# Kernel tuning notes

Hardware: AMD Instinct MI355X
Metric: run time of the kernel (lower is better)

Reference implementation:

```python
import jax, jax.numpy as jnp
import numpy as np

H = 2048          # hidden_size
I = 1024          # moe_intermediate_size
E = 32            # n_routed_experts
K = 4             # num_experts_per_tok
N_SHARED = 1
EPS = 1e-6


def setup_inputs() -> dict:
    key = jax.random.key(0)
    ks = jax.random.split(key, 8)
    s = 1.0 / np.sqrt(H)
    si = 1.0 / np.sqrt(I)
    return {
        "hidden_states": jax.random.normal(ks[0], (1, 4096, H), jnp.float32),
        "norm_w": jnp.ones((H,), jnp.float32),
        "gate_w": jax.random.normal(ks[1], (E, H), jnp.float32) * s,      # MoEGate.weight
        "w13": jax.random.normal(ks[2], (E, H, 2 * I), jnp.float32) * s,  # fused w1w3
        "w2": jax.random.normal(ks[3], (E, I, H), jnp.float32) * si,      # fused w2
        "shared_gate_w": jax.random.normal(ks[4], (H, I * N_SHARED), jnp.float32) * s,
        "shared_up_w": jax.random.normal(ks[5], (H, I * N_SHARED), jnp.float32) * s,
        "shared_down_w": jax.random.normal(ks[6], (I * N_SHARED, H), jnp.float32) * si,
    }


def _rmsnorm(x, w, eps=EPS):
    var = jnp.mean(jnp.square(x), axis=-1, keepdims=True)
    return x * jax.lax.rsqrt(var + eps) * w


def _moe_core(x, gate_w, w13, w2):
    # x: [T, H] (post-norm tokens)
    T = x.shape[0]
    N = T * K
    C = 2 * N // E

    # --- gate (fp32, F.linear) ---
    logits = jnp.einsum("th,eh->te", x.astype(jnp.float32), gate_w.astype(jnp.float32))
    scores = jax.nn.softmax(logits, axis=-1)
    topk_w, topk_ids = jax.lax.top_k(scores, K)           # [T, K]
    topk_w = topk_w / jnp.sum(topk_w, axis=-1, keepdims=True)  # norm_topk_prob

    # --- dispatch: sort token-expert pairs by expert ---
    flat_ids = topk_ids.reshape(-1)                        # [N] int
    flat_w = topk_w.reshape(-1)                            # [N]
    order = jnp.argsort(flat_ids)                          # stable sort by expert
    sorted_eid = flat_ids[order]                           # [N]
    tok = order // K                                       # source token per sorted slot
    counts = jnp.zeros((E,), jnp.int32).at[flat_ids].add(1)  # tokens_per_expert
    starts = jnp.cumsum(counts) - counts
    pos = jnp.arange(N) - starts[sorted_eid]               # position within expert group

    # scatter tokens into [E, C, H] buffer (OOB rows dropped; C sized so this ~never happens)
    buf = jnp.zeros((E, C, x.shape[1]), x.dtype).at[sorted_eid, pos].set(x[tok], mode="drop")

    # --- grouped expert FFN (swiglu) ---
    gu = jnp.einsum("ech,ehf->ecf", buf, w13)              # [E, C, 2I]
    g, u = jnp.split(gu, 2, axis=-1)
    act = jax.nn.silu(g) * u                               # swiglu
    eo = jnp.einsum("eci,eih->ech", act, w2)               # [E, C, H]

    # --- combine: gather back and weighted scatter-add per source token ---
    out_slots = eo[sorted_eid, pos]                        # [N, H]
    routed = jnp.zeros_like(x).at[tok].add(out_slots * flat_w[order][:, None])
    return routed


def reference(hidden_states, norm_w, gate_w, w13, w2, shared_gate_w, shared_up_w, shared_down_w):
    B, S, Hd = hidden_states.shape
    residual = hidden_states
    h = _rmsnorm(hidden_states, norm_w)                    # post_attention_layernorm
    x = h.reshape(-1, Hd)                                  # [T, H]

    routed = _moe_core(x, gate_w, w13, w2)                 # routed experts output

    # shared experts MLP (swiglu)
    shared = (jax.nn.silu(x @ shared_gate_w) * (x @ shared_up_w)) @ shared_down_w

    out = residual + (routed + shared).reshape(B, S, Hd)
    return out
```

## Files before the change

kernel.cpp:

```cpp
#include <hip/hip_runtime.h>
#include <hip/hip_bf16.h>
#include <math.h>

#define HD 2048
#define ID 1024
#define NE 32
#define TOPK 4
#define NTOK 4096
#define NSLOT (NTOK*TOPK)

typedef __attribute__((ext_vector_type(4))) float f32x4;
typedef __attribute__((ext_vector_type(8))) short bf16x8;
typedef unsigned short u16;
typedef unsigned int u32;

union U32x4BF { uint4 u; bf16x8 h; };

static __device__ __forceinline__ u16 f2bf(float f) {
  union { float f; u32 u; } v; v.f = f;
  u32 r = v.u + 0x7fffu + ((v.u >> 16) & 1u);
  return (u16)(r >> 16);
}

static __device__ __forceinline__ u32 cvtpk(float lo, float hi) {
  u32 r;
  asm("v_cvt_pk_bf16_f32 %0, %1, %2" : "=v"(r) : "v"(lo), "v"(hi));
  return r;
}

static __device__ __forceinline__ void barrier_lgkm() {
  asm volatile("s_waitcnt lgkmcnt(0)" ::: "memory");
  __builtin_amdgcn_s_barrier();
}

__global__ __launch_bounds__(256) void k_rmsnorm(const float* __restrict__ x,
                                                 const float* __restrict__ w,
                                                 u16* __restrict__ xn) {
  int t = blockIdx.x, tid = threadIdx.x;
  const float* row = x + (size_t)t * HD;
  float4 v0 = ((const float4*)row)[tid*2+0];
  float4 v1 = ((const float4*)row)[tid*2+1];
  float ss = v0.x*v0.x+v0.y*v0.y+v0.z*v0.z+v0.w*v0.w
           + v1.x*v1.x+v1.y*v1.y+v1.z*v1.z+v1.w*v1.w;
  #pragma unroll
  for (int d=1; d<64; d<<=1) ss += __shfl_xor(ss, d);
  __shared__ float red[4];
  if ((tid&63)==0) red[tid>>6] = ss;
  __syncthreads();
  float rs = rsqrtf((red[0]+red[1]+red[2]+red[3]) * (1.0f/HD) + 1e-6f);
  const float* wp = w + tid*8;
  float a[8] = {v0.x,v0.y,v0.z,v0.w,v1.x,v1.y,v1.z,v1.w};
  uint4 o;
  o.x = (u32)f2bf(a[0]*rs*wp[0]) | ((u32)f2bf(a[1]*rs*wp[1])<<16);
  o.y = (u32)f2bf(a[2]*rs*wp[2]) | ((u32)f2bf(a[3]*rs*wp[3])<<16);
  o.z = (u32)f2bf(a[4]*rs*wp[4]) | ((u32)f2bf(a[5]*rs*wp[5])<<16);
  o.w = (u32)f2bf(a[6]*rs*wp[6]) | ((u32)f2bf(a[7]*rs*wp[7])<<16);
  ((uint4*)xn)[(size_t)t*(HD/8) + tid] = o;
}

__global__ __launch_bounds__(256) void k_gate(const float* __restrict__ x,
                                              const float* __restrict__ w,
                                              const float* __restrict__ gw,
                                              int* __restrict__ topk_id,
                                              float* __restrict__ topk_w,
                                              int* __restrict__ counts) {
  __shared__ float xs[HD];
  __shared__ float red[4];
  __shared__ float logits[NE];
  int t = blockIdx.x, tid = threadIdx.x;
  const float* row = x + (size_t)t*HD;
  float4 v0 = ((const float4*)row)[tid*2+0];
  float4 v1 = ((const float4*)row)[tid*2+1];
  float ss = v0.x*v0.x+v0.y*v0.y+v0.z*v0.z+v0.w*v0.w
           + v1.x*v1.x+v1.y*v1.y+v1.z*v1.z+v1.w*v1.w;
  #pragma unroll
  for (int d=1; d<64; d<<=1) ss += __shfl_xor(ss, d);
  if ((tid&63)==0) red[tid>>6] = ss;
  __syncthreads();
  float rs = 1.0f / sqrtf((red[0]+red[1]+red[2]+red[3]) * (1.0f/HD) + 1e-6f);
  const float* wp = w + tid*8;
  float a[8] = {v0.x,v0.y,v0.z,v0.w,v1.x,v1.y,v1.z,v1.w};
  #pragma unroll
  for (int j=0;j<8;++j) xs[tid*8+j] = a[j]*rs*wp[j];
  __syncthreads();
  int wave = tid>>6, lane = tid&63;
  for (int ei=0; ei<8; ++ei) {
    int e = wave*8 + ei;
    const float* g = gw + (size_t)e*HD;
    float s = 0.f;
    #pragma unroll
    for (int j=0;j<HD/64;++j) s += xs[lane + j*64] * g[lane + j*64];
    #pragma unroll
    for (int d=1; d<64; d<<=1) s += __shfl_xor(s, d);
    if (lane==0) logits[e] = s;
  }
  __syncthreads();
  if (tid==0) {
    float best[TOPK]; int bid[TOPK]; unsigned used = 0;
    for (int k2=0;k2<TOPK;++k2) {
      float bv = -1e30f; int bi = 0;
      for (int i2=0;i2<NE;++i2)
        if (!((used>>i2)&1u) && logits[i2] > bv) { bv = logits[i2]; bi = i2; }
      used |= 1u<<bi; best[k2] = bv; bid[k2] = bi;
    }
    float mx = best[0], sum = 0.f, wv[TOPK];
    for (int k2=0;k2<TOPK;++k2) { wv[k2] = expf(best[k2]-mx); sum += wv[k2]; }
    float inv = 1.f/sum;
    for (int k2=0;k2<TOPK;++k2) {
      topk_id[t*TOPK+k2] = bid[k2];
      topk_w[t*TOPK+k2] = wv[k2]*inv;
      atomicAdd(&counts[bid[k2]], 1);
    }
  }
}

__global__ void k_zero(int* counts, int* cursors) {
  int i = threadIdx.x;
  if (i < NE) { counts[i] = 0; cursors[i] = 0; }
}

__global__ void k_scan(const int* __restrict__ counts, int* __restrict__ starts) {
  if (threadIdx.x==0 && blockIdx.x==0) {
    int acc = 0;
    for (int e=0;e<NE;++e) { starts[e] = acc; acc += counts[e]; }
  }
}

__global__ __launch_bounds__(256) void k_dispatch(const int* __restrict__ topk_id,
                                                  const float* __restrict__ topk_w,
                                                  const int* __restrict__ starts,
                                                  int* __restrict__ cursors,
                                                  int* __restrict__ slot_tok,
                                                  float* __restrict__ slot_w) {
  int i = blockIdx.x*256 + threadIdx.x;
  int e = topk_id[i];
  int p = atomicAdd(&cursors[e], 1);
  int slot = starts[e] + p;
  slot_tok[slot] = i >> 2;
  slot_w[slot] = topk_w[i];
}

template<bool INDEXED>
__global__ __launch_bounds__(256) void k_gemm_up(
    const u16* __restrict__ A, int lda, int kiter,
    const float* __restrict__ Bg, const float* __restrict__ Bu,
    size_t bstride, int ldb,
    const int* __restrict__ counts, const int* __restrict__ starts,
    const int* __restrict__ slot_tok,
    u16* __restrict__ actOut) {
  __shared__ u16 Al[2][4096];
  __shared__ u16 Bl[2][4096];
  __shared__ int rowL[128];
  int t = threadIdx.x;
  int n0 = blockIdx.x * 64;
  int m0 = blockIdx.y * 128;
  int e  = blockIdx.z;
  int M, rowbase;
  if (INDEXED) { M = counts[e]; rowbase = starts[e]; if (m0 >= M) return; }
  else { M = NTOK; rowbase = 0; }
  if (t < 128) {
    int m = m0 + t;
    rowL[t] = INDEXED ? slot_tok[rowbase + (m < M ? m : M-1)] : m;
  }
  __syncthreads();
  int r0i = t>>2, r1i = r0i + 64;
  int segA = ((t&3) ^ ((r0i>>1)&3)) << 3;
  const u16* srcA0 = A + (size_t)rowL[r0i]*lda + segA;
  const u16* srcA1 = A + (size_t)rowL[r1i]*lda + segA;
  int sc4 = (t&31)*4;
  int kb  = t>>5;
  int isup = (sc4>>4)&1;
  int srccol = n0 + ((sc4>>5)<<4) + (sc4&15);
  const float* bsrc = (isup ? Bu : Bg) + (INDEXED ? (size_t)e*bstride : 0)
                    + (size_t)(kb*4)*ldb + srccol;
  int bq4 = (kb ^ (t&7))*4;

  int lane = t&63, wave = t>>6, wr = wave>>1, wc = wave&1;
  int l15 = lane&15, l4 = lane>>4;
  int aoff[4], b0off[4], b1off[4];
  #pragma unroll
  for (int f=0; f<4; ++f) {
    int r = wr*64 + f*16 + l15;
    aoff[f] = r*32 + ((l4 ^ ((r>>1)&3))<<3);
    int c = wc*64 + f*16 + l15;
    int g = (c>>2)&7;
    b0off[f] = c*32 + (((2*l4)   ^ g)<<2);
    b1off[f] = c*32 + (((2*l4+1) ^ g)<<2);
  }
  f32x4 acc[4][4];
  #pragma unroll
  for (int fm=0;fm<4;++fm)
    #pragma unroll
    for (int fn=0;fn<4;++fn)
      acc[fm][fn] = (f32x4){0.f,0.f,0.f,0.f};

  uint4 av0 = *(const uint4*)srcA0;
  uint4 av1 = *(const uint4*)srcA1;
  float4 bv[4];
  #pragma unroll
  for (int i=0;i<4;++i) bv[i] = *(const float4*)(bsrc + (size_t)i*ldb);
  srcA0 += 32; srcA1 += 32; bsrc += (size_t)32*ldb;
  *(uint4*)&Al[0][t*8] = av0;
  *(uint4*)&Al[0][2048 + t*8] = av1;
  {
    const float* f0 = (const float*)&bv[0];
    const float* f1 = (const float*)&bv[1];
    const float* f2 = (const float*)&bv[2];
    const float* f3 = (const float*)&bv[3];
    #pragma unroll
    for (int j=0;j<4;++j) {
      uint2 wv; wv.x = cvtpk(f0[j], f1[j]); wv.y = cvtpk(f2[j], f3[j]);
      *(uint2*)&Bl[0][(sc4+j)*32 + bq4] = wv;
    }
  }
  barrier_lgkm();

  int cur = 0;
  for (int kt = 0; kt < kiter; ++kt) {
    bool more = (kt+1 < kiter);
    uint4 avn0, avn1; float4 bvn[4];
    if (more) {
      avn0 = *(const uint4*)srcA0;
      avn1 = *(const uint4*)srcA1;
      #pragma unroll
      for (int i=0;i<4;++i) bvn[i] = *(const float4*)(bsrc + (size_t)i*ldb);
      srcA0 += 32; srcA1 += 32; bsrc += (size_t)32*ldb;
    }
    bf16x8 af[4], bfr[4];
    #pragma unroll
    for (int f=0; f<4; ++f) af[f] = *(const bf16x8*)&Al[cur][aoff[f]];
    #pragma unroll
    for (int f=0; f<4; ++f) {
      uint2 lo = *(const uint2*)&Bl[cur][b0off[f]];
      uint2 hi = *(const uint2*)&Bl[cur][b1off[f]];
      U32x4BF ub; ub.u = make_uint4(lo.x, lo.y, hi.x, hi.y);
      bfr[f] = ub.h;
    }
    #pragma unroll
    for (int fm=0; fm<4; ++fm)
      #pragma unroll
      for (int fn=0; fn<4; ++fn)
        acc[fm][fn] = __builtin_amdgcn_mfma_f32_16x16x32_bf16(af[fm], bfr[fn], acc[fm][fn], 0,0,0);
    if (more) {
      *(uint4*)&Al[cur^1][t*8] = avn0;
      *(uint4*)&Al[cur^1][2048 + t*8] = avn1;
      const float* f0 = (const float*)&bvn[0];
      const float* f1 = (const float*)&bvn[1];
      const float* f2 = (const float*)&bvn[2];
      const float* f3 = (const float*)&bvn[3];
      #pragma unroll
      for (int j=0;j<4;++j) {
        uint2 wv; wv.x = cvtpk(f0[j], f1[j]); wv.y = cvtpk(f2[j], f3[j]);
        *(uint2*)&Bl[cur^1][(sc4+j)*32 + bq4] = wv;
      }
    }
    cur ^= 1;
    barrier_lgkm();
  }
  #pragma unroll
  for (int fm=0; fm<4; ++fm) {
    #pragma unroll
    for (int fq=0; fq<2; ++fq) {
      f32x4 g = acc[fm][2*fq], u = acc[fm][2*fq+1];
      int col = n0 + (wc*2+fq)*16 + l15;
      #pragma unroll
      for (int r=0;r<4;++r) {
        int mloc = wr*64 + fm*16 + l4*4 + r;
        int m = m0 + mloc;
        if (m < M) {
          float gv = g[r];
          float av = gv / (1.f + expf(-gv)) * u[r];
          actOut[(size_t)(rowbase+m)*ID + col] = f2bf(av);
        }
      }
    }
  }
}

template<bool INDEXED>
__global__ __launch_bounds__(256) void k_gemm_down(
    const u16* __restrict__ A, int lda, int kiter,
    const float* __restrict__ B, size_t bstride, int ldb,
    const int* __restrict__ counts, const int* __restrict__ starts,
    const int* __restrict__ slot_tok, const float* __restrict__ slot_w,
    const float* __restrict__ resid,
    float* __restrict__ out) {
  __shared__ u16 Al[2][4096];
  __shared__ u16 Bl[2][4096];
  __shared__ int tokL[128];
  __shared__ float wL[128];
  int t = threadIdx.x;
  int n0 = blockIdx.x * 128;
  int m0 = blockIdx.y * 128;
  int e  = blockIdx.z;
  int M, rowbase;
  if (INDEXED) { M = counts[e]; rowbase = starts[e]; if (m0 >= M) return; }
  else { M = NTOK; rowbase = 0; }
  if (INDEXED && t < 128) {
    int m = m0 + t;
    tokL[t] = (m<M) ? slot_tok[rowbase+m] : 0;
    wL[t]   = (m<M) ? slot_w[rowbase+m]  : 0.f;
  }
  if (INDEXED) __syncthreads();
  int r0i = t>>2, r1i = r0i + 64;
  int segA = ((t&3) ^ ((r0i>>1)&3)) << 3;
  int am0 = m0 + r0i, am1 = m0 + r1i;
  const u16* srcA0 = A + (size_t)(rowbase + (am0 < M ? am0 : M-1))*lda + segA;
  const u16* srcA1 = A + (size_t)(rowbase + (am1 < M ? am1 : M-1))*lda + segA;
  int sc4 = (t&31)*4;
  int kb  = t>>5;
  const float* bsrc = B + (INDEXED ? (size_t)e*bstride : 0)
                    + (size_t)(kb*4)*ldb + (n0 + sc4);
  int bq4 = (kb ^ (t&7))*4;

  int lane = t&63, wave = t>>6, wr = wave>>1, wc = wave&1;
  int l15 = lane&15, l4 = lane>>4;
  int aoff[4], b0off[4], b1off[4];
  #pragma unroll
  for (int f=0; f<4; ++f) {
    int r = wr*64 + f*16 + l15;
    aoff[f] = r*32 + ((l4 ^ ((r>>1)&3))<<3);
    int c = wc*64 + f*16 + l15;
    int g = (c>>2)&7;
    b0off[f] = c*32 + (((2*l4)   ^ g)<<2);
    b1off[f] = c*32 + (((2*l4+1) ^ g)<<2);
  }
  f32x4 acc[4][4];
  #pragma unroll
  for (int fm=0;fm<4;++fm)
    #pragma unroll
    for (int fn=0;fn<4;++fn)
      acc[fm][fn] = (f32x4){0.f,0.f,0.f,0.f};

  uint4 av0 = *(const uint4*)srcA0;
  uint4 av1 = *(const uint4*)srcA1;
  float4 bv[4];
  #pragma unroll
  for (int i=0;i<4;++i) bv[i] = *(const float4*)(bsrc + (size_t)i*ldb);
  srcA0 += 32; srcA1 += 32; bsrc += (size_t)32*ldb;
  *(uint4*)&Al[0][t*8] = av0;
  *(uint4*)&Al[0][2048 + t*8] = av1;
  {
    const float* f0 = (const float*)&bv[0];
    const float* f1 = (const float*)&bv[1];
    const float* f2 = (const float*)&bv[2];
    const float* f3 = (const float*)&bv[3];
    #pragma unroll
    for (int j=0;j<4;++j) {
      uint2 wv; wv.x = cvtpk(f0[j], f1[j]); wv.y = cvtpk(f2[j], f3[j]);
      *(uint2*)&Bl[0][(sc4+j)*32 + bq4] = wv;
    }
  }
  barrier_lgkm();

  int cur = 0;
  for (int kt = 0; kt < kiter; ++kt) {
    bool more = (kt+1 < kiter);
    uint4 avn0, avn1; float4 bvn[4];
    if (more) {
      avn0 = *(const uint4*)srcA0;
      avn1 = *(const uint4*)srcA1;
      #pragma unroll
      for (int i=0;i<4;++i) bvn[i] = *(const float4*)(bsrc + (size_t)i*ldb);
      srcA0 += 32; srcA1 += 32; bsrc += (size_t)32*ldb;
    }
    bf16x8 af[4], bfr[4];
    #pragma unroll
    for (int f=0; f<4; ++f) af[f] = *(const bf16x8*)&Al[cur][aoff[f]];
    #pragma unroll
    for (int f=0; f<4; ++f) {
      uint2 lo = *(const uint2*)&Bl[cur][b0off[f]];
      uint2 hi = *(const uint2*)&Bl[cur][b1off[f]];
      U32x4BF ub; ub.u = make_uint4(lo.x, lo.y, hi.x, hi.y);
      bfr[f] = ub.h;
    }
    #pragma unroll
    for (int fm=0; fm<4; ++fm)
      #pragma unroll
      for (int fn=0; fn<4; ++fn)
        acc[fm][fn] = __builtin_amdgcn_mfma_f32_16x16x32_bf16(af[fm], bfr[fn], acc[fm][fn], 0,0,0);
    if (more) {
      *(uint4*)&Al[cur^1][t*8] = avn0;
      *(uint4*)&Al[cur^1][2048 + t*8] = avn1;
      const float* f0 = (const float*)&bvn[0];
      const float* f1 = (const float*)&bvn[1];
      const float* f2 = (const float*)&bvn[2];
      const float* f3 = (const float*)&bvn[3];
      #pragma unroll
      for (int j=0;j<4;++j) {
        uint2 wv; wv.x = cvtpk(f0[j], f1[j]); wv.y = cvtpk(f2[j], f3[j]);
        *(uint2*)&Bl[cur^1][(sc4+j)*32 + bq4] = wv;
      }
    }
    cur ^= 1;
    barrier_lgkm();
  }
  #pragma unroll
  for (int fm=0; fm<4; ++fm) {
    #pragma unroll
    for (int fn=0; fn<4; ++fn) {
      f32x4 v = acc[fm][fn];
      int col = n0 + wc*64 + fn*16 + l15;
      #pragma unroll
      for (int r=0;r<4;++r) {
        int mloc = wr*64 + fm*16 + l4*4 + r;
        int m = m0 + mloc;
        if (m < M) {
          if (INDEXED) {
            atomicAdd(&out[(size_t)tokL[mloc]*HD + col], v[r]*wL[mloc]);
          } else {
            size_t o = (size_t)m*HD + col;
            out[o] = resid[o] + v[r];
          }
        }
      }
    }
  }
}

extern "C" void kernel_launch(void* const* d_in, const int* in_sizes, int n_in,
                              void* d_out, int out_size, void* d_ws, size_t ws_size,
                              hipStream_t stream) {
  const float* x    = (const float*)d_in[0];
  const float* nw   = (const float*)d_in[1];
  const float* gw   = (const float*)d_in[2];
  const float* w13  = (const float*)d_in[3];
  const float* w2   = (const float*)d_in[4];
  const float* sgw  = (const float*)d_in[5];
  const float* suw  = (const float*)d_in[6];
  const float* sdw  = (const float*)d_in[7];
  float* out = (float*)d_out;

  char* p = (char*)d_ws;
  u16* xn   = (u16*)p;  p += (size_t)NTOK*HD*2;
  u16* act  = (u16*)p;  p += (size_t)NSLOT*ID*2;
  u16* sact = (u16*)p;  p += (size_t)NTOK*ID*2;
  int*   topk_id  = (int*)p;   p += (size_t)NTOK*TOPK*4;
  float* topk_w   = (float*)p; p += (size_t)NTOK*TOPK*4;
  int*   slot_tok = (int*)p;   p += (size_t)NSLOT*4;
  float* slot_w   = (float*)p; p += (size_t)NSLOT*4;
  int*   counts   = (int*)p;   p += 64*4;
  int*   cursors  = (int*)p;   p += 64*4;
  int*   starts   = (int*)p;   p += 64*4;

  k_zero<<<1, 64, 0, stream>>>(counts, cursors);
  k_rmsnorm<<<NTOK, 256, 0, stream>>>(x, nw, xn);
  k_gate<<<NTOK, 256, 0, stream>>>(x, nw, gw, topk_id, topk_w, counts);
  k_scan<<<1, 1, 0, stream>>>(counts, starts);
  k_dispatch<<<NSLOT/256, 256, 0, stream>>>(topk_id, topk_w, starts, cursors, slot_tok, slot_w);

  k_gemm_up<true><<<dim3(ID/64, 8, NE), 256, 0, stream>>>(
      xn, HD, HD/32, w13, w13 + ID, (size_t)HD*2*ID, 2*ID,
      counts, starts, slot_tok, act);
  k_gemm_up<false><<<dim3(ID/64, NTOK/128, 1), 256, 0, stream>>>(
      xn, HD, HD/32, sgw, suw, 0, ID, nullptr, nullptr, nullptr, sact);
  k_gemm_down<false><<<dim3(HD/128, NTOK/128, 1), 256, 0, stream>>>(
      sact, ID, ID/32, sdw, 0, HD, nullptr, nullptr, nullptr, nullptr, x, out);
  k_gemm_down<true><<<dim3(HD/128, 8, NE), 256, 0, stream>>>(
      act, ID, ID/32, w2, (size_t)ID*HD, HD, counts, starts, slot_tok, slot_w, nullptr, out);
}
```

Before: 792.2 us.

## Double N tile width in MoE GEMMs with per-wave column split and new LDS swizzle

New measurement: 869.6 us. 9.8% more time.

```diff
diff --git a/kernel.cpp b/kernel.cpp
--- a/kernel.cpp
+++ b/kernel.cpp
@@ -140,8 +140,31 @@
   slot_w[slot] = topk_w[i];
 }
 
+static __device__ __forceinline__ void packB(u16* Bb, int tq, int kb, const float4* bv) {
+  int h = tq & 15;
+  #pragma unroll
+  for (int j = 0; j < 4; ++j) {
+    int p = 2*tq + (j>>1);
+    int cpar = j & 1;
+    int s0 = ((4*kb + 0 + cpar) ^ h) * 4;
+    int s1 = ((4*kb + 2 + cpar) ^ h) * 4;
+    uint2 w0, w1;
+    w0.x = cvtpk(((const float*)&bv[0])[j], ((const float*)&bv[1])[j]);
+    w0.y = cvtpk(((const float*)&bv[2])[j], ((const float*)&bv[3])[j]);
+    w1.x = cvtpk(((const float*)&bv[4])[j], ((const float*)&bv[5])[j]);
+    w1.y = cvtpk(((const float*)&bv[6])[j], ((const float*)&bv[7])[j]);
+    *(uint2*)&Bb[p*64 + s0] = w0;
+    *(uint2*)&Bb[p*64 + s1] = w1;
+  }
+}
+
+static __device__ __forceinline__ void loadB8(const float* bsrc, int ldb, float4* bv) {
+  #pragma unroll
+  for (int i = 0; i < 8; ++i) bv[i] = *(const float4*)(bsrc + (size_t)i*ldb);
+}
+
 template<bool INDEXED>
-__global__ __launch_bounds__(256) void k_gemm_up(
+__global__ __launch_bounds__(256, 2) void k_gemm_up(
     const u16* __restrict__ A, int lda, int kiter,
     const float* __restrict__ Bg, const float* __restrict__ Bu,
     size_t bstride, int ldb,
@@ -149,10 +172,10 @@
     const int* __restrict__ slot_tok,
     u16* __restrict__ actOut) {
   __shared__ u16 Al[2][4096];
-  __shared__ u16 Bl[2][4096];
+  __shared__ u16 Bl[2][8192];
   __shared__ int rowL[128];
   int t = threadIdx.x;
-  int n0 = blockIdx.x * 64;
+  int n0 = blockIdx.x * 128;
   int m0 = blockIdx.y * 128;
   int e  = blockIdx.z;
   int M, rowbase;
@@ -163,109 +186,86 @@
     rowL[t] = INDEXED ? slot_tok[rowbase + (m < M ? m : M-1)] : m;
   }
   __syncthreads();
-  int r0i = t>>2, r1i = r0i + 64;
+  int r0i = t>>2;
   int segA = ((t&3) ^ ((r0i>>1)&3)) << 3;
   const u16* srcA0 = A + (size_t)rowL[r0i]*lda + segA;
-  const u16* srcA1 = A + (size_t)rowL[r1i]*lda + segA;
-  int sc4 = (t&31)*4;
-  int kb  = t>>5;
-  int isup = (sc4>>4)&1;
-  int srccol = n0 + ((sc4>>5)<<4) + (sc4&15);
+  const u16* srcA1 = A + (size_t)rowL[r0i+64]*lda + segA;
+  int tq = t & 63, kb = t >> 6;
+  int sc4 = tq * 4;
+  int isup = (sc4 >> 4) & 1;
+  int og = ((sc4 >> 5) << 4) | (sc4 & 15);
   const float* bsrc = (isup ? Bu : Bg) + (INDEXED ? (size_t)e*bstride : 0)
-                    + (size_t)(kb*4)*ldb + srccol;
-  int bq4 = (kb ^ (t&7))*4;
-
-  int lane = t&63, wave = t>>6, wr = wave>>1, wc = wave&1;
+                    + (size_t)(kb*8)*ldb + (n0 + og);
+
+  int lane = t&63, wn = t>>6;
   int l15 = lane&15, l4 = lane>>4;
-  int aoff[4], b0off[4], b1off[4];
-  #pragma unroll
-  for (int f=0; f<4; ++f) {
-    int r = wr*64 + f*16 + l15;
-    aoff[f] = r*32 + ((l4 ^ ((r>>1)&3))<<3);
-    int c = wc*64 + f*16 + l15;
-    int g = (c>>2)&7;
-    b0off[f] = c*32 + (((2*l4)   ^ g)<<2);
-    b1off[f] = c*32 + (((2*l4+1) ^ g)<<2);
-  }
-  f32x4 acc[4][4];
-  #pragma unroll
-  for (int fm=0;fm<4;++fm)
+  int aoffb = l15*32 + ((l4 ^ ((l15>>1)&3))<<3);
+  int b0off[4];
+  #pragma unroll
+  for (int fn=0; fn<4; ++fn) {
+    int pbase = wn*32 + fn*8 + (l15>>1);
+    int h = (fn*4 + (l15>>2)) & 15;
+    b0off[fn] = pbase*64 + (((4*l4 + (l15&1)) ^ h) << 2);
+  }
+  f32x4 acc[8][4];
+  #pragma unroll
+  for (int fm=0;fm<8;++fm)
     #pragma unroll
     for (int fn=0;fn<4;++fn)
       acc[fm][fn] = (f32x4){0.f,0.f,0.f,0.f};
 
-  uint4 av0 = *(const uint4*)srcA0;
-  uint4 av1 = *(const uint4*)srcA1;
-  float4 bv[4];
-  #pragma unroll
-  for (int i=0;i<4;++i) bv[i] = *(const float4*)(bsrc + (size_t)i*ldb);
+  uint4 aA0 = *(const uint4*)srcA0, aA1 = *(const uint4*)srcA1;
+  float4 bv[8]; loadB8(bsrc, ldb, bv);
   srcA0 += 32; srcA1 += 32; bsrc += (size_t)32*ldb;
-  *(uint4*)&Al[0][t*8] = av0;
-  *(uint4*)&Al[0][2048 + t*8] = av1;
-  {
-    const float* f0 = (const float*)&bv[0];
-    const float* f1 = (const float*)&bv[1];
-    const float* f2 = (const float*)&bv[2];
-    const float* f3 = (const float*)&bv[3];
-    #pragma unroll
-    for (int j=0;j<4;++j) {
-      uint2 wv; wv.x = cvtpk(f0[j], f1[j]); wv.y = cvtpk(f2[j], f3[j]);
-      *(uint2*)&Bl[0][(sc4+j)*32 + bq4] = wv;
-    }
-  }
+  *(uint4*)&Al[0][t*8] = aA0;
+  *(uint4*)&Al[0][2048 + t*8] = aA1;
+  packB(Bl[0], tq, kb, bv);
   barrier_lgkm();
 
   int cur = 0;
   for (int kt = 0; kt < kiter; ++kt) {
     bool more = (kt+1 < kiter);
-    uint4 avn0, avn1; float4 bvn[4];
     if (more) {
-      avn0 = *(const uint4*)srcA0;
-      avn1 = *(const uint4*)srcA1;
-      #pragma unroll
-      for (int i=0;i<4;++i) bvn[i] = *(const float4*)(bsrc + (size_t)i*ldb);
+      aA0 = *(const uint4*)srcA0; aA1 = *(const uint4*)srcA1;
+      loadB8(bsrc, ldb, bv);
       srcA0 += 32; srcA1 += 32; bsrc += (size_t)32*ldb;
     }
-    bf16x8 af[4], bfr[4];
-    #pragma unroll
-    for (int f=0; f<4; ++f) af[f] = *(const bf16x8*)&Al[cur][aoff[f]];
-    #pragma unroll
-    for (int f=0; f<4; ++f) {
-      uint2 lo = *(const uint2*)&Bl[cur][b0off[f]];
-      uint2 hi = *(const uint2*)&Bl[cur][b1off[f]];
-      U32x4BF ub; ub.u = make_uint4(lo.x, lo.y, hi.x, hi.y);
-      bfr[f] = ub.h;
-    }
-    #pragma unroll
-    for (int fm=0; fm<4; ++fm)
-      #pragma unroll
-      for (int fn=0; fn<4; ++fn)
-        acc[fm][fn] = __builtin_amdgcn_mfma_f32_16x16x32_bf16(af[fm], bfr[fn], acc[fm][fn], 0,0,0);
+    {
+      bf16x8 bfr[4];
+      #pragma unroll
+      for (int fn=0; fn<4; ++fn) {
+        uint2 lo = *(const uint2*)&Bl[cur][b0off[fn]];
+        uint2 hi = *(const uint2*)&Bl[cur][b0off[fn] ^ 8];
+        U32x4BF ub; ub.u = make_uint4(lo.x, lo.y, hi.x, hi.y);
+        bfr[fn] = ub.h;
+      }
+      __builtin_amdgcn_s_setprio(1);
+      #pragma unroll
+      for (int fm=0; fm<8; ++fm) {
+        bf16x8 af = *(const bf16x8*)&Al[cur][aoffb + fm*512];
+        #pragma unroll
+        for (int fn=0; fn<4; ++fn)
+          acc[fm][fn] = __builtin_amdgcn_mfma_f32_16x16x32_bf16(af, bfr[fn], acc[fm][fn], 0,0,0);
+      }
+      __builtin_amdgcn_s_setprio(0);
+    }
     if (more) {
-      *(uint4*)&Al[cur^1][t*8] = avn0;
-      *(uint4*)&Al[cur^1][2048 + t*8] = avn1;
-      const float* f0 = (const float*)&bvn[0];
-      const float* f1 = (const float*)&bvn[1];
-      const float* f2 = (const float*)&bvn[2];
-      const float* f3 = (const float*)&bvn[3];
-      #pragma unroll
-      for (int j=0;j<4;++j) {
-        uint2 wv; wv.x = cvtpk(f0[j], f1[j]); wv.y = cvtpk(f2[j], f3[j]);
-        *(uint2*)&Bl[cur^1][(sc4+j)*32 + bq4] = wv;
-      }
+      *(uint4*)&Al[cur^1][t*8] = aA0;
+      *(uint4*)&Al[cur^1][2048 + t*8] = aA1;
+      packB(Bl[cur^1], tq, kb, bv);
     }
     cur ^= 1;
     barrier_lgkm();
   }
   #pragma unroll
-  for (int fm=0; fm<4; ++fm) {
+  for (int fm=0; fm<8; ++fm) {
     #pragma unroll
     for (int fq=0; fq<2; ++fq) {
       f32x4 g = acc[fm][2*fq], u = acc[fm][2*fq+1];
-      int col = n0 + (wc*2+fq)*16 + l15;
+      int col = n0 + (wn*2+fq)*16 + l15;
       #pragma unroll
       for (int r=0;r<4;++r) {
-        int mloc = wr*64 + fm*16 + l4*4 + r;
+        int mloc = fm*16 + l4*4 + r;
         int m = m0 + mloc;
         if (m < M) {
           float gv = g[r];
@@ -278,7 +278,7 @@
 }
 
 template<bool INDEXED>
-__global__ __launch_bounds__(256) void k_gemm_down(
+__global__ __launch_bounds__(256, 2) void k_gemm_down(
     const u16* __restrict__ A, int lda, int kiter,
     const float* __restrict__ B, size_t bstride, int ldb,
     const int* __restrict__ counts, const int* __restrict__ starts,
@@ -286,11 +286,11 @@
     const float* __restrict__ resid,
     float* __restrict__ out) {
   __shared__ u16 Al[2][4096];
-  __shared__ u16 Bl[2][4096];
+  __shared__ u16 Bl[2][8192];
   __shared__ int tokL[128];
   __shared__ float wL[128];
   int t = threadIdx.x;
-  int n0 = blockIdx.x * 128;
+  int n0 = blockIdx.x * 256;
   int m0 = blockIdx.y * 128;
   int e  = blockIdx.z;
   int M, rowbase;
@@ -302,108 +302,85 @@
     wL[t]   = (m<M) ? slot_w[rowbase+m]  : 0.f;
   }
   if (INDEXED) __syncthreads();
-  int r0i = t>>2, r1i = r0i + 64;
+  int r0i = t>>2;
   int segA = ((t&3) ^ ((r0i>>1)&3)) << 3;
-  int am0 = m0 + r0i, am1 = m0 + r1i;
+  int am0 = m0 + r0i, am1 = m0 + r0i + 64;
   const u16* srcA0 = A + (size_t)(rowbase + (am0 < M ? am0 : M-1))*lda + segA;
   const u16* srcA1 = A + (size_t)(rowbase + (am1 < M ? am1 : M-1))*lda + segA;
-  int sc4 = (t&31)*4;
-  int kb  = t>>5;
+  int tq = t & 63, kb = t >> 6;
+  int sc4 = tq * 4;
   const float* bsrc = B + (INDEXED ? (size_t)e*bstride : 0)
-                    + (size_t)(kb*4)*ldb + (n0 + sc4);
-  int bq4 = (kb ^ (t&7))*4;
-
-  int lane = t&63, wave = t>>6, wr = wave>>1, wc = wave&1;
+                    + (size_t)(kb*8)*ldb + (n0 + sc4);
+
+  int lane = t&63, wn = t>>6;
   int l15 = lane&15, l4 = lane>>4;
-  int aoff[4], b0off[4], b1off[4];
-  #pragma unroll
-  for (int f=0; f<4; ++f) {
-    int r = wr*64 + f*16 + l15;
-    aoff[f] = r*32 + ((l4 ^ ((r>>1)&3))<<3);
-    int c = wc*64 + f*16 + l15;
-    int g = (c>>2)&7;
-    b0off[f] = c*32 + (((2*l4)   ^ g)<<2);
-    b1off[f] = c*32 + (((2*l4+1) ^ g)<<2);
-  }
-  f32x4 acc[4][4];
-  #pragma unroll
-  for (int fm=0;fm<4;++fm)
+  int aoffb = l15*32 + ((l4 ^ ((l15>>1)&3))<<3);
+  int b0off[4];
+  #pragma unroll
+  for (int fn=0; fn<4; ++fn) {
+    int pbase = wn*32 + fn*8 + (l15>>1);
+    int h = (fn*4 + (l15>>2)) & 15;
+    b0off[fn] = pbase*64 + (((4*l4 + (l15&1)) ^ h) << 2);
+  }
+  f32x4 acc[8][4];
+  #pragma unroll
+  for (int fm=0;fm<8;++fm)
     #pragma unroll
     for (int fn=0;fn<4;++fn)
       acc[fm][fn] = (f32x4){0.f,0.f,0.f,0.f};
 
-  uint4 av0 = *(const uint4*)srcA0;
-  uint4 av1 = *(const uint4*)srcA1;
-  float4 bv[4];
-  #pragma unroll
-  for (int i=0;i<4;++i) bv[i] = *(const float4*)(bsrc + (size_t)i*ldb);
+  uint4 aA0 = *(const uint4*)srcA0, aA1 = *(const uint4*)srcA1;
+  float4 bv[8]; loadB8(bsrc, ldb, bv);
   srcA0 += 32; srcA1 += 32; bsrc += (size_t)32*ldb;
-  *(uint4*)&Al[0][t*8] = av0;
-  *(uint4*)&Al[0][2048 + t*8] = av1;
-  {
-    const float* f0 = (const float*)&bv[0];
-    const float* f1 = (const float*)&bv[1];
-    const float* f2 = (const float*)&bv[2];
-    const float* f3 = (const float*)&bv[3];
-    #pragma unroll
-    for (int j=0;j<4;++j) {
-      uint2 wv; wv.x = cvtpk(f0[j], f1[j]); wv.y = cvtpk(f2[j], f3[j]);
-      *(uint2*)&Bl[0][(sc4+j)*32 + bq4] = wv;
-    }
-  }
+  *(uint4*)&Al[0][t*8] = aA0;
+  *(uint4*)&Al[0][2048 + t*8] = aA1;
+  packB(Bl[0], tq, kb, bv);
   barrier_lgkm();
 
   int cur = 0;
   for (int kt = 0; kt < kiter; ++kt) {
     bool more = (kt+1 < kiter);
-    uint4 avn0, avn1; float4 bvn[4];
     if (more) {
-      avn0 = *(const uint4*)srcA0;
-      avn1 = *(const uint4*)srcA1;
-      #pragma unroll
-      for (int i=0;i<4;++i) bvn[i] = *(const float4*)(bsrc + (size_t)i*ldb);
+      aA0 = *(const uint4*)srcA0; aA1 = *(const uint4*)srcA1;
+      loadB8(bsrc, ldb, bv);
       srcA0 += 32; srcA1 += 32; bsrc += (size_t)32*ldb;
     }
-    bf16x8 af[4], bfr[4];
-    #pragma unroll
-    for (int f=0; f<4; ++f) af[f] = *(const bf16x8*)&Al[cur][aoff[f]];
-    #pragma unroll
-    for (int f=0; f<4; ++f) {
-      uint2 lo = *(const uint2*)&Bl[cur][b0off[f]];
-      uint2 hi = *(const uint2*)&Bl[cur][b1off[f]];
-      U32x4BF ub; ub.u = make_uint4(lo.x, lo.y, hi.x, hi.y);
-      bfr[f] = ub.h;
-    }
-    #pragma unroll
-    for (int fm=0; fm<4; ++fm)
-      #pragma unroll
-      for (int fn=0; fn<4; ++fn)
-        acc[fm][fn] = __builtin_amdgcn_mfma_f32_16x16x32_bf16(af[fm], bfr[fn], acc[fm][fn], 0,0,0);
+    {
+      bf16x8 bfr[4];
+      #pragma unroll
+      for (int fn=0; fn<4; ++fn) {
+        uint2 lo = *(const uint2*)&Bl[cur][b0off[fn]];
+        uint2 hi = *(const uint2*)&Bl[cur][b0off[fn] ^ 8];
+        U32x4BF ub; ub.u = make_uint4(lo.x, lo.y, hi.x, hi.y);
+        bfr[fn] = ub.h;
+      }
+      __builtin_amdgcn_s_setprio(1);
+      #pragma unroll
+      for (int fm=0; fm<8; ++fm) {
+        bf16x8 af = *(const bf16x8*)&Al[cur][aoffb + fm*512];
+        #pragma unroll
+        for (int fn=0; fn<4; ++fn)
+          acc[fm][fn] = __builtin_amdgcn_mfma_f32_16x16x32_bf16(af, bfr[fn], acc[fm][fn], 0,0,0);
+      }
+      __builtin_amdgcn_s_setprio(0);
+    }
     if (more) {
-      *(uint4*)&Al[cur^1][t*8] = avn0;
-      *(uint4*)&Al[cur^1][2048 + t*8] = avn1;
-      const float* f0 = (const float*)&bvn[0];
-      const float* f1 = (const float*)&bvn[1];
-      const float* f2 = (const float*)&bvn[2];
-      const float* f3 = (const float*)&bvn[3];
-      #pragma unroll
-      for (int j=0;j<4;++j) {
-        uint2 wv; wv.x = cvtpk(f0[j], f1[j]); wv.y = cvtpk(f2[j], f3[j]);
-        *(uint2*)&Bl[cur^1][(sc4+j)*32 + bq4] = wv;
-      }
+      *(uint4*)&Al[cur^1][t*8] = aA0;
+      *(uint4*)&Al[cur^1][2048 + t*8] = aA1;
+      packB(Bl[cur^1], tq, kb, bv);
     }
     cur ^= 1;
     barrier_lgkm();
   }
   #pragma unroll
-  for (int fm=0; fm<4; ++fm) {
+  for (int fm=0; fm<8; ++fm) {
     #pragma unroll
     for (int fn=0; fn<4; ++fn) {
       f32x4 v = acc[fm][fn];
-      int col = n0 + wc*64 + fn*16 + l15;
+      int col = n0 + wn*64 + fn*16 + l15;
       #pragma unroll
       for (int r=0;r<4;++r) {
-        int mloc = wr*64 + fm*16 + l4*4 + r;
+        int mloc = fm*16 + l4*4 + r;
         int m = m0 + mloc;
         if (m < M) {
           if (INDEXED) {
@@ -449,13 +426,13 @@
   k_scan<<<1, 1, 0, stream>>>(counts, starts);
   k_dispatch<<<NSLOT/256, 256, 0, stream>>>(topk_id, topk_w, starts, cursors, slot_tok, slot_w);
 
-  k_gemm_up<true><<<dim3(ID/64, 8, NE), 256, 0, stream>>>(
+  k_gemm_up<true><<<dim3(ID/128, 8, NE), 256, 0, stream>>>(
       xn, HD, HD/32, w13, w13 + ID, (size_t)HD*2*ID, 2*ID,
       counts, starts, slot_tok, act);
-  k_gemm_up<false><<<dim3(ID/64, NTOK/128, 1), 256, 0, stream>>>(
+  k_gemm_up<false><<<dim3(ID/128, NTOK/128, 1), 256, 0, stream>>>(
       xn, HD, HD/32, sgw, suw, 0, ID, nullptr, nullptr, nullptr, sact);
-  k_gemm_down<false><<<dim3(HD/128, NTOK/128, 1), 256, 0, stream>>>(
+  k_gemm_down<false><<<dim3(HD/256, NTOK/128, 1), 256, 0, stream>>>(
       sact, ID, ID/32, sdw, 0, HD, nullptr, nullptr, nullptr, nullptr, x, out);
-  k_gemm_down<true><<<dim3(HD/128, 8, NE), 256, 0, stream>>>(
+  k_gemm_down<true><<<dim3(HD/256, 8, NE), 256, 0, stream>>>(
       act, ID, ID/32, w2, (size_t)ID*HD, HD, counts, starts, slot_tok, slot_w, nullptr, out);
 }
```
